# Kernel tuning notes

Hardware: AMD Instinct MI355X
Metric: run time of the kernel (lower is better)

## Reference

```python
import jax, jax.numpy as jnp
import numpy as np
import math

D, DK, DV = 1024, 128, 128
B, S = 4, 2048

def setup_inputs() -> dict:
    key = jax.random.key(0)
    k1, k2, k3, k4 = jax.random.split(key, 4)
    # xavier_normal std = sqrt(2/(fan_in+fan_out))
    std_qk = math.sqrt(2.0 / (D + DK))
    std_v = math.sqrt(2.0 / (D + DV))
    return {
        "X": jax.random.normal(k1, (B, S, D), dtype=jnp.float32),
        "W_q": jax.random.normal(k2, (D, DK), dtype=jnp.float32) * std_qk,
        "W_k": jax.random.normal(k3, (D, DK), dtype=jnp.float32) * std_qk,
        "W_v": jax.random.normal(k4, (D, DV), dtype=jnp.float32) * std_v,
    }

def reference(X, W_q, W_k, W_v):
    # Q,K,V projections: [B,S,D] @ [D,dk] -> [B,S,dk]
    Q = X @ W_q
    K = X @ W_k
    V = X @ W_v
    scale = 1.0 / math.sqrt(DK)
    # NOTE: original torch code calls A.masked_fill(...) without assigning the
    # result, so the causal mask is never actually applied. We replicate the
    # executed math: unmasked scaled dot-product attention.
    A = jnp.einsum("bqd,bkd->bqk", Q, K) * scale  # [B,S,S]
    A = jax.nn.softmax(A, axis=2)
    return jnp.einsum("bqk,bkv->bqv", A, V)  # [B,S,DV]
```

## Files before the change

### kernel.cpp

```cpp
#include <hip/hip_runtime.h>
#include <stdint.h>
#include <math.h>


typedef __attribute__((ext_vector_type(4))) float  f32x4;
typedef __attribute__((ext_vector_type(4))) short  s16x4;
typedef __attribute__((ext_vector_type(8))) short  s16x8;
typedef __attribute__((ext_vector_type(4))) float  fl4;

#define MFMA16(a,b,c) __builtin_amdgcn_mfma_f32_16x16x16bf16_1k(a,b,c,0,0,0)
#define MFMA32(a,b,c) __builtin_amdgcn_mfma_f32_16x16x32_bf16(a,b,c,0,0,0)

__device__ __forceinline__ short f2bf(float f){
  uint32_t u = __builtin_bit_cast(uint32_t, f);
  u = (u + 0x7FFFu + ((u >> 16) & 1u)) >> 16;
  return (short)u;
}

#define S_LEN   2048
#define D_IN    1024
#define D_HEAD  128
#define NROWS   8192
#define NSPLIT  4
#define KVB     64
#define KVPER   (S_LEN / NSPLIT)
#define NT      (KVPER / KVB)

#define WT_OFF  0u
#define Q_OFF   786432u
#define K_OFF   (786432u + 2097152u)
#define V_OFF   (786432u + 2u*2097152u)
#define OP_OFF  (786432u + 3u*2097152u)
#define ML_OFF  (OP_OFF + 16777216u)

__global__ __launch_bounds__(256) void wt3_kernel(
    const float* __restrict__ Wq, const float* __restrict__ Wk,
    const float* __restrict__ Wv, short* __restrict__ Wt){
  int i = blockIdx.x * 256 + threadIdx.x;
  int m = i >> 17;
  int r = i & 131071;
  int n = r >> 10;
  int k = r & 1023;
  const float* W = (m == 0) ? Wq : (m == 1 ? Wk : Wv);
  float v = W[k * D_HEAD + n];
  if (m == 0) v *= 0.08838834764831845f;
  Wt[i] = f2bf(v);
}

__global__ __launch_bounds__(256) void proj_kernel(
    const float* __restrict__ X, const short* __restrict__ Wt,
    short* __restrict__ Qo, short* __restrict__ Ko, short* __restrict__ Vt){
  const int mt  = blockIdx.x;
  const int mat = blockIdx.y;
  const short* Wm = Wt + mat * 131072;

  __shared__ short Xs[32][72];
  __shared__ short Ws[128][72];

  const int tid  = threadIdx.x;
  const int lane = tid & 63;
  const int wid  = tid >> 6;
  const int wm   = (wid >> 1) * 16;
  const int wn   = (wid & 1) * 64;
  const int lr   = lane & 15;
  const int lg8  = (lane >> 4) * 8;

  const f32x4 zero4 = {0.f, 0.f, 0.f, 0.f};
  f32x4 acc[4];
  #pragma unroll
  for (int n = 0; n < 4; n++) acc[n] = zero4;

  const int xr = tid >> 3, xc = (tid & 7) * 8;
  const int wr = tid >> 1, wc = (tid & 1) * 32;

  const float* xsrc0 = X + (size_t)(mt * 32 + xr) * D_IN + xc;
  const short* wsrc0 = Wm + (size_t)wr * D_IN + wc;

  fl4   xA, xB;
  s16x8 wR[4];

  xA = *(const fl4*)(xsrc0);
  xB = *(const fl4*)(xsrc0 + 4);
  #pragma unroll
  for (int j = 0; j < 4; j++) wR[j] = *(const s16x8*)(wsrc0 + 8 * j);

  #pragma unroll 1
  for (int kt = 0; kt < D_IN; kt += 64){
    {
      s16x8 v;
      #pragma unroll
      for (int j = 0; j < 4; j++){ v[j] = f2bf(xA[j]); v[j+4] = f2bf(xB[j]); }
      *(s16x8*)&Xs[xr][xc] = v;
      #pragma unroll
      for (int j = 0; j < 4; j++) *(s16x8*)&Ws[wr][wc + 8*j] = wR[j];
    }
    __syncthreads();

    if (kt + 64 < D_IN){
      xA = *(const fl4*)(xsrc0 + kt + 64);
      xB = *(const fl4*)(xsrc0 + kt + 68);
      #pragma unroll
      for (int j = 0; j < 4; j++) wR[j] = *(const s16x8*)(wsrc0 + kt + 64 + 8*j);
    }

    #pragma unroll
    for (int kc = 0; kc < 64; kc += 32){
      s16x8 af = *(const s16x8*)&Xs[wm + lr][kc + lg8];
      #pragma unroll
      for (int n = 0; n < 4; n++){
        s16x8 bf = *(const s16x8*)&Ws[wn + n*16 + lr][kc + lg8];
        acc[n] = MFMA32(af, bf, acc[n]);
      }
    }
    __syncthreads();
  }

  const int lg4 = (lane >> 4) * 4;
  if (mat < 2){
    short* dst = (mat == 0) ? Qo : Ko;
    #pragma unroll
    for (int n = 0; n < 4; n++){
      int col = wn + n*16 + lr;
      #pragma unroll
      for (int r = 0; r < 4; r++){
        int row = mt*32 + wm + lg4 + r;
        dst[(size_t)row * D_HEAD + col] = f2bf(acc[n][r]);
      }
    }
  } else {
    const int b  = (mt * 32) >> 11;
    const int s0 = (mt * 32) & 2047;
    #pragma unroll
    for (int n = 0; n < 4; n++){
      int dv = wn + n*16 + lr;
      int s  = s0 + wm + lg4;
      s16x4 v;
      #pragma unroll
      for (int r = 0; r < 4; r++) v[r] = f2bf(acc[n][r]);
      *(s16x4*)&Vt[((size_t)b * D_HEAD + dv) * S_LEN + s] = v;
    }
  }
}

__global__ __launch_bounds__(256) void flash_kernel(
    const short* __restrict__ Q, const short* __restrict__ K,
    const short* __restrict__ Vt, float* __restrict__ Opart,
    float* __restrict__ MLpart){
  const int sp = blockIdx.x;
  const int qt = blockIdx.y;
  const int b  = blockIdx.z;

  __shared__ short Ks[KVB][136];
  __shared__ short Vs[128][72];

  const int tid  = threadIdx.x;
  const int lane = tid & 63;
  const int w    = tid >> 6;
  const int lr   = lane & 15;
  const int lg   = lane >> 4;

  const int qrow = qt * 64 + w * 16 + lr;
  const short* Qr = Q + (size_t)(b * S_LEN + qrow) * D_HEAD + 8 * lg;
  s16x8 qf[4];
  #pragma unroll
  for (int c = 0; c < 4; c++) qf[c] = *(const s16x8*)(Qr + c * 32);

  const f32x4 zero4 = {0.f, 0.f, 0.f, 0.f};
  f32x4 o[8];
  #pragma unroll
  for (int t = 0; t < 8; t++) o[t] = zero4;
  float m_run = -INFINITY, l_run = 0.0f;

  const short* Kb = K  + (size_t)b * S_LEN * D_HEAD;
  const short* Vb = Vt + (size_t)b * D_HEAD * S_LEN;
  const int kr = tid >> 2, kc = (tid & 3) * 32;
  const int vr = tid >> 1, vc = (tid & 1) * 32;

  s16x8 kR[4], vR[4];
  const int kv_beg = sp * KVPER;

  {
    const short* ks = Kb + (size_t)(kv_beg + kr) * D_HEAD + kc;
    const short* vs = Vb + (size_t)vr * S_LEN + kv_beg + vc;
    #pragma unroll
    for (int j = 0; j < 4; j++){
      kR[j] = *(const s16x8*)(ks + 8*j);
      vR[j] = *(const s16x8*)(vs + 8*j);
    }
  }
  #pragma unroll
  for (int j = 0; j < 4; j++){
    *(s16x8*)&Ks[kr][kc + 8*j] = kR[j];
    *(s16x8*)&Vs[vr][vc + 8*j] = vR[j];
  }
  __syncthreads();

  #pragma unroll 1
  for (int it = 0; it < NT; ++it){
    if (it + 1 < NT){
      int kv0 = kv_beg + (it + 1) * KVB;
      const short* ks = Kb + (size_t)(kv0 + kr) * D_HEAD + kc;
      const short* vs = Vb + (size_t)vr * S_LEN + kv0 + vc;
      #pragma unroll
      for (int j = 0; j < 4; j++){
        kR[j] = *(const s16x8*)(ks + 8*j);
        vR[j] = *(const s16x8*)(vs + 8*j);
      }
    }

    f32x4 sa[4];
    #pragma unroll
    for (int t = 0; t < 4; t++) sa[t] = zero4;
    #pragma unroll
    for (int c = 0; c < 4; c++){
      #pragma unroll
      for (int t = 0; t < 4; t++){
        s16x8 ka = *(const s16x8*)&Ks[t*16 + lr][c*32 + 8*lg];
        sa[t] = MFMA32(ka, qf[c], sa[t]);
      }
    }

    float p[16]; float mx = -INFINITY;
    #pragma unroll
    for (int t = 0; t < 4; t++)
      #pragma unroll
      for (int r = 0; r < 4; r++){
        p[t*4 + r] = sa[t][r];
        mx = fmaxf(mx, sa[t][r]);
      }
    mx = fmaxf(mx, __shfl_xor(mx, 16));
    mx = fmaxf(mx, __shfl_xor(mx, 32));
    if (!__all(mx <= m_run + 8.0f)){
      float m_new = fmaxf(m_run, mx);
      float alpha = __expf(m_run - m_new);
      l_run *= alpha;
      #pragma unroll
      for (int t = 0; t < 8; t++) o[t] *= alpha;
      m_run = m_new;
    }
    float lsum = 0.0f;
    #pragma unroll
    for (int j = 0; j < 16; j++){ p[j] = __expf(p[j] - m_run); lsum += p[j]; }
    lsum += __shfl_xor(lsum, 16);
    lsum += __shfl_xor(lsum, 32);
    l_run += lsum;

    s16x4 pb[4];
    #pragma unroll
    for (int t = 0; t < 4; t++)
      #pragma unroll
      for (int r = 0; r < 4; r++) pb[t][r] = f2bf(p[t*4 + r]);

    #pragma unroll
    for (int dt = 0; dt < 8; dt++){
      #pragma unroll
      for (int t = 0; t < 4; t++){
        s16x4 va = *(const s16x4*)&Vs[dt*16 + lr][t*16 + 4*lg];
        o[dt] = MFMA16(va, pb[t], o[dt]);
      }
    }

    if (it + 1 < NT){
      __syncthreads();
      #pragma unroll
      for (int j = 0; j < 4; j++){
        *(s16x8*)&Ks[kr][kc + 8*j] = kR[j];
        *(s16x8*)&Vs[vr][vc + 8*j] = vR[j];
      }
      __syncthreads();
    }
  }

  const size_t grow = (size_t)b * S_LEN + qrow;
  float* Op = Opart + ((size_t)sp * NROWS + grow) * D_HEAD + 4 * lg;
  #pragma unroll
  for (int dt = 0; dt < 8; dt++)
    *(f32x4*)(Op + dt * 16) = o[dt];
  if (lg == 0){
    float* ml = MLpart + ((size_t)sp * NROWS + grow) * 2;
    ml[0] = m_run; ml[1] = l_run;
  }
}

__global__ __launch_bounds__(256) void merge_kernel(
    const float* __restrict__ Opart, const float* __restrict__ MLpart,
    float* __restrict__ out){
  int idx = blockIdx.x * 256 + threadIdx.x;
  int row = idx >> 7;
  float m[NSPLIT], l[NSPLIT];
  float M = -INFINITY;
  #pragma unroll
  for (int s = 0; s < NSPLIT; s++){
    m[s] = MLpart[((size_t)s * NROWS + row) * 2 + 0];
    l[s] = MLpart[((size_t)s * NROWS + row) * 2 + 1];
    M = fmaxf(M, m[s]);
  }
  float L = 0.f, val = 0.f;
  #pragma unroll
  for (int s = 0; s < NSPLIT; s++){
    float e = __expf(m[s] - M);
    L   += l[s] * e;
    val += Opart[(size_t)s * NROWS * D_HEAD + idx] * e;
  }
  out[idx] = val / L;
}

extern "C" void kernel_launch(void* const* d_in, const int* in_sizes, int n_in,
                              void* d_out, int out_size, void* d_ws, size_t ws_size,
                              hipStream_t stream){
  const float* X  = (const float*)d_in[0];
  const float* Wq = (const float*)d_in[1];
  const float* Wk = (const float*)d_in[2];
  const float* Wv = (const float*)d_in[3];
  char* ws = (char*)d_ws;
  short* Wt = (short*)(ws + WT_OFF);
  short* Qp = (short*)(ws + Q_OFF);
  short* Kp = (short*)(ws + K_OFF);
  short* Vt = (short*)(ws + V_OFF);
  float* Op = (float*)(ws + OP_OFF);
  float* Ml = (float*)(ws + ML_OFF);
  float* out = (float*)d_out;

  wt3_kernel  <<<dim3(1536),          dim3(256), 0, stream>>>(Wq, Wk, Wv, Wt);
  proj_kernel <<<dim3(256, 3),        dim3(256), 0, stream>>>(X, Wt, Qp, Kp, Vt);
  flash_kernel<<<dim3(NSPLIT, 32, 4), dim3(256), 0, stream>>>(Qp, Kp, Vt, Op, Ml);
  merge_kernel<<<dim3(4096),          dim3(256), 0, stream>>>(Op, Ml, out);
}
```

Before: 128.6 us.

## Double per-warp query rows in flash and projection, split KV into eight, use exp2

Each flash warp now handles two 16-row query fragments (128-row Q block), so every K and V fragment read from LDS feeds two MFMAs. KV is split eight ways to keep the grid size similar. The projection kernel likewise computes two M fragments per warp, reusing each W fragment twice. log2(e) is folded into the Q weight so softmax can use exp2f. s_setprio is raised around the MFMA sections. The cost is more accumulator registers per thread and twice the partial output traffic through the merge.

```diff
diff --git a/kernel.cpp b/kernel.cpp
--- a/kernel.cpp
+++ b/kernel.cpp
@@ -21,17 +21,21 @@
 #define D_IN    1024
 #define D_HEAD  128
 #define NROWS   8192
-#define NSPLIT  4
+#define NSPLIT  8
 #define KVB     64
 #define KVPER   (S_LEN / NSPLIT)
 #define NT      (KVPER / KVB)
+#define QBLK    128
 
 #define WT_OFF  0u
 #define Q_OFF   786432u
 #define K_OFF   (786432u + 2097152u)
 #define V_OFF   (786432u + 2u*2097152u)
 #define OP_OFF  (786432u + 3u*2097152u)
-#define ML_OFF  (OP_OFF + 16777216u)
+#define ML_OFF  (OP_OFF + 33554432u)
+
+#define LOG2E   1.4426950408889634f
+#define DEFER_TH 11.541560327111708f
 
 __global__ __launch_bounds__(256) void wt3_kernel(
     const float* __restrict__ Wq, const float* __restrict__ Wk,
@@ -43,7 +47,7 @@
   int k = r & 1023;
   const float* W = (m == 0) ? Wq : (m == 1 ? Wk : Wv);
   float v = W[k * D_HEAD + n];
-  if (m == 0) v *= 0.08838834764831845f;
+  if (m == 0) v *= 0.08838834764831845f * LOG2E;
   Wt[i] = f2bf(v);
 }
 
@@ -54,62 +58,75 @@
   const int mat = blockIdx.y;
   const short* Wm = Wt + mat * 131072;
 
-  __shared__ short Xs[32][72];
+  __shared__ short Xs[64][72];
   __shared__ short Ws[128][72];
 
   const int tid  = threadIdx.x;
   const int lane = tid & 63;
   const int wid  = tid >> 6;
-  const int wm   = (wid >> 1) * 16;
+  const int wm   = (wid >> 1) * 32;
   const int wn   = (wid & 1) * 64;
   const int lr   = lane & 15;
   const int lg8  = (lane >> 4) * 8;
 
   const f32x4 zero4 = {0.f, 0.f, 0.f, 0.f};
-  f32x4 acc[4];
-  #pragma unroll
-  for (int n = 0; n < 4; n++) acc[n] = zero4;
-
-  const int xr = tid >> 3, xc = (tid & 7) * 8;
+  f32x4 acc[2][4];
+  #pragma unroll
+  for (int mf = 0; mf < 2; mf++)
+    #pragma unroll
+    for (int n = 0; n < 4; n++) acc[mf][n] = zero4;
+
+  const int xr = tid >> 2, xc = (tid & 3) * 16;
   const int wr = tid >> 1, wc = (tid & 1) * 32;
 
-  const float* xsrc0 = X + (size_t)(mt * 32 + xr) * D_IN + xc;
+  const float* xsrc0 = X + (size_t)(mt * 64 + xr) * D_IN + xc;
   const short* wsrc0 = Wm + (size_t)wr * D_IN + wc;
 
-  fl4   xA, xB;
+  fl4   xA[4];
   s16x8 wR[4];
 
-  xA = *(const fl4*)(xsrc0);
-  xB = *(const fl4*)(xsrc0 + 4);
-  #pragma unroll
-  for (int j = 0; j < 4; j++) wR[j] = *(const s16x8*)(wsrc0 + 8 * j);
+  #pragma unroll
+  for (int j = 0; j < 4; j++){
+    xA[j] = *(const fl4*)(xsrc0 + 4 * j);
+    wR[j] = *(const s16x8*)(wsrc0 + 8 * j);
+  }
 
   #pragma unroll 1
   for (int kt = 0; kt < D_IN; kt += 64){
     {
-      s16x8 v;
-      #pragma unroll
-      for (int j = 0; j < 4; j++){ v[j] = f2bf(xA[j]); v[j+4] = f2bf(xB[j]); }
-      *(s16x8*)&Xs[xr][xc] = v;
+      s16x8 v0, v1;
+      #pragma unroll
+      for (int j = 0; j < 4; j++){
+        v0[j] = f2bf(xA[0][j]); v0[j+4] = f2bf(xA[1][j]);
+        v1[j] = f2bf(xA[2][j]); v1[j+4] = f2bf(xA[3][j]);
+      }
+      *(s16x8*)&Xs[xr][xc]     = v0;
+      *(s16x8*)&Xs[xr][xc + 8] = v1;
       #pragma unroll
       for (int j = 0; j < 4; j++) *(s16x8*)&Ws[wr][wc + 8*j] = wR[j];
     }
     __syncthreads();
 
     if (kt + 64 < D_IN){
-      xA = *(const fl4*)(xsrc0 + kt + 64);
-      xB = *(const fl4*)(xsrc0 + kt + 68);
-      #pragma unroll
-      for (int j = 0; j < 4; j++) wR[j] = *(const s16x8*)(wsrc0 + kt + 64 + 8*j);
+      #pragma unroll
+      for (int j = 0; j < 4; j++){
+        xA[j] = *(const fl4*)(xsrc0 + kt + 64 + 4*j);
+        wR[j] = *(const s16x8*)(wsrc0 + kt + 64 + 8*j);
+      }
     }
 
     #pragma unroll
     for (int kc = 0; kc < 64; kc += 32){
-      s16x8 af = *(const s16x8*)&Xs[wm + lr][kc + lg8];
+      s16x8 af[2];
+      #pragma unroll
+      for (int mf = 0; mf < 2; mf++)
+        af[mf] = *(const s16x8*)&Xs[wm + mf*16 + lr][kc + lg8];
       #pragma unroll
       for (int n = 0; n < 4; n++){
         s16x8 bf = *(const s16x8*)&Ws[wn + n*16 + lr][kc + lg8];
-        acc[n] = MFMA32(af, bf, acc[n]);
+        #pragma unroll
+        for (int mf = 0; mf < 2; mf++)
+          acc[mf][n] = MFMA32(af[mf], bf, acc[mf][n]);
       }
     }
     __syncthreads();
@@ -119,26 +136,30 @@
   if (mat < 2){
     short* dst = (mat == 0) ? Qo : Ko;
     #pragma unroll
-    for (int n = 0; n < 4; n++){
-      int col = wn + n*16 + lr;
-      #pragma unroll
-      for (int r = 0; r < 4; r++){
-        int row = mt*32 + wm + lg4 + r;
-        dst[(size_t)row * D_HEAD + col] = f2bf(acc[n][r]);
-      }
-    }
+    for (int mf = 0; mf < 2; mf++)
+      #pragma unroll
+      for (int n = 0; n < 4; n++){
+        int col = wn + n*16 + lr;
+        #pragma unroll
+        for (int r = 0; r < 4; r++){
+          int row = mt*64 + wm + mf*16 + lg4 + r;
+          dst[(size_t)row * D_HEAD + col] = f2bf(acc[mf][n][r]);
+        }
+      }
   } else {
-    const int b  = (mt * 32) >> 11;
-    const int s0 = (mt * 32) & 2047;
-    #pragma unroll
-    for (int n = 0; n < 4; n++){
-      int dv = wn + n*16 + lr;
-      int s  = s0 + wm + lg4;
-      s16x4 v;
-      #pragma unroll
-      for (int r = 0; r < 4; r++) v[r] = f2bf(acc[n][r]);
-      *(s16x4*)&Vt[((size_t)b * D_HEAD + dv) * S_LEN + s] = v;
-    }
+    const int b  = (mt * 64) >> 11;
+    const int s0 = (mt * 64) & 2047;
+    #pragma unroll
+    for (int mf = 0; mf < 2; mf++)
+      #pragma unroll
+      for (int n = 0; n < 4; n++){
+        int dv = wn + n*16 + lr;
+        int s  = s0 + wm + mf*16 + lg4;
+        s16x4 v;
+        #pragma unroll
+        for (int r = 0; r < 4; r++) v[r] = f2bf(acc[mf][n][r]);
+        *(s16x4*)&Vt[((size_t)b * D_HEAD + dv) * S_LEN + s] = v;
+      }
   }
 }
 
@@ -159,17 +180,23 @@
   const int lr   = lane & 15;
   const int lg   = lane >> 4;
 
-  const int qrow = qt * 64 + w * 16 + lr;
-  const short* Qr = Q + (size_t)(b * S_LEN + qrow) * D_HEAD + 8 * lg;
-  s16x8 qf[4];
-  #pragma unroll
-  for (int c = 0; c < 4; c++) qf[c] = *(const s16x8*)(Qr + c * 32);
+  const int qrow0 = qt * QBLK + w * 32 + lr;
+  const short* Qr = Q + (size_t)(b * S_LEN + qrow0) * D_HEAD + 8 * lg;
+  s16x8 qf[2][4];
+  #pragma unroll
+  for (int qi = 0; qi < 2; qi++)
+    #pragma unroll
+    for (int c = 0; c < 4; c++)
+      qf[qi][c] = *(const s16x8*)(Qr + qi * 16 * D_HEAD + c * 32);
 
   const f32x4 zero4 = {0.f, 0.f, 0.f, 0.f};
-  f32x4 o[8];
-  #pragma unroll
-  for (int t = 0; t < 8; t++) o[t] = zero4;
-  float m_run = -INFINITY, l_run = 0.0f;
+  f32x4 o[2][8];
+  #pragma unroll
+  for (int qi = 0; qi < 2; qi++)
+    #pragma unroll
+    for (int t = 0; t < 8; t++) o[qi][t] = zero4;
+  float m_run[2] = {-INFINITY, -INFINITY};
+  float l_run[2] = {0.0f, 0.0f};
 
   const short* Kb = K  + (size_t)b * S_LEN * D_HEAD;
   const short* Vb = Vt + (size_t)b * D_HEAD * S_LEN;
@@ -208,57 +235,66 @@
       }
     }
 
-    f32x4 sa[4];
-    #pragma unroll
-    for (int t = 0; t < 4; t++) sa[t] = zero4;
+    f32x4 sa[2][4];
+    #pragma unroll
+    for (int qi = 0; qi < 2; qi++)
+      #pragma unroll
+      for (int t = 0; t < 4; t++) sa[qi][t] = zero4;
+    __builtin_amdgcn_s_setprio(1);
     #pragma unroll
     for (int c = 0; c < 4; c++){
       #pragma unroll
       for (int t = 0; t < 4; t++){
         s16x8 ka = *(const s16x8*)&Ks[t*16 + lr][c*32 + 8*lg];
-        sa[t] = MFMA32(ka, qf[c], sa[t]);
-      }
-    }
-
-    float p[16]; float mx = -INFINITY;
-    #pragma unroll
-    for (int t = 0; t < 4; t++)
-      #pragma unroll
-      for (int r = 0; r < 4; r++){
-        p[t*4 + r] = sa[t][r];
-        mx = fmaxf(mx, sa[t][r]);
-      }
-    mx = fmaxf(mx, __shfl_xor(mx, 16));
-    mx = fmaxf(mx, __shfl_xor(mx, 32));
-    if (!__all(mx <= m_run + 8.0f)){
-      float m_new = fmaxf(m_run, mx);
-      float alpha = __expf(m_run - m_new);
-      l_run *= alpha;
-      #pragma unroll
-      for (int t = 0; t < 8; t++) o[t] *= alpha;
-      m_run = m_new;
-    }
-    float lsum = 0.0f;
-    #pragma unroll
-    for (int j = 0; j < 16; j++){ p[j] = __expf(p[j] - m_run); lsum += p[j]; }
-    lsum += __shfl_xor(lsum, 16);
-    lsum += __shfl_xor(lsum, 32);
-    l_run += lsum;
-
-    s16x4 pb[4];
-    #pragma unroll
-    for (int t = 0; t < 4; t++)
-      #pragma unroll
-      for (int r = 0; r < 4; r++) pb[t][r] = f2bf(p[t*4 + r]);
-
+        sa[0][t] = MFMA32(ka, qf[0][c], sa[0][t]);
+        sa[1][t] = MFMA32(ka, qf[1][c], sa[1][t]);
+      }
+    }
+    __builtin_amdgcn_s_setprio(0);
+
+    s16x4 pb[2][4];
+    #pragma unroll
+    for (int qi = 0; qi < 2; qi++){
+      float mx = -INFINITY;
+      #pragma unroll
+      for (int t = 0; t < 4; t++)
+        #pragma unroll
+        for (int r = 0; r < 4; r++) mx = fmaxf(mx, sa[qi][t][r]);
+      mx = fmaxf(mx, __shfl_xor(mx, 16));
+      mx = fmaxf(mx, __shfl_xor(mx, 32));
+      if (!__all(mx <= m_run[qi] + DEFER_TH)){
+        float m_new = fmaxf(m_run[qi], mx);
+        float alpha = exp2f(m_run[qi] - m_new);
+        l_run[qi] *= alpha;
+        #pragma unroll
+        for (int t = 0; t < 8; t++) o[qi][t] *= alpha;
+        m_run[qi] = m_new;
+      }
+      float lsum = 0.0f;
+      #pragma unroll
+      for (int t = 0; t < 4; t++)
+        #pragma unroll
+        for (int r = 0; r < 4; r++){
+          float e = exp2f(sa[qi][t][r] - m_run[qi]);
+          pb[qi][t][r] = f2bf(e);
+          lsum += e;
+        }
+      lsum += __shfl_xor(lsum, 16);
+      lsum += __shfl_xor(lsum, 32);
+      l_run[qi] += lsum;
+    }
+
+    __builtin_amdgcn_s_setprio(1);
     #pragma unroll
     for (int dt = 0; dt < 8; dt++){
       #pragma unroll
       for (int t = 0; t < 4; t++){
         s16x4 va = *(const s16x4*)&Vs[dt*16 + lr][t*16 + 4*lg];
-        o[dt] = MFMA16(va, pb[t], o[dt]);
-      }
-    }
+        o[0][dt] = MFMA16(va, pb[0][t], o[0][dt]);
+        o[1][dt] = MFMA16(va, pb[1][t], o[1][dt]);
+      }
+    }
+    __builtin_amdgcn_s_setprio(0);
 
     if (it + 1 < NT){
       __syncthreads();
@@ -271,14 +307,18 @@
     }
   }
 
-  const size_t grow = (size_t)b * S_LEN + qrow;
-  float* Op = Opart + ((size_t)sp * NROWS + grow) * D_HEAD + 4 * lg;
-  #pragma unroll
-  for (int dt = 0; dt < 8; dt++)
-    *(f32x4*)(Op + dt * 16) = o[dt];
-  if (lg == 0){
-    float* ml = MLpart + ((size_t)sp * NROWS + grow) * 2;
-    ml[0] = m_run; ml[1] = l_run;
+  const int lg4 = lg * 4;
+  #pragma unroll
+  for (int qi = 0; qi < 2; qi++){
+    const size_t grow = (size_t)b * S_LEN + qrow0 + qi * 16;
+    float* Op = Opart + ((size_t)sp * NROWS + grow) * D_HEAD + lg4;
+    #pragma unroll
+    for (int dt = 0; dt < 8; dt++)
+      *(f32x4*)(Op + dt * 16) = o[qi][dt];
+    if (lg == 0){
+      float* ml = MLpart + ((size_t)sp * NROWS + grow) * 2;
+      ml[0] = m_run[qi]; ml[1] = l_run[qi];
+    }
   }
 }
 
@@ -298,7 +338,7 @@
   float L = 0.f, val = 0.f;
   #pragma unroll
   for (int s = 0; s < NSPLIT; s++){
-    float e = __expf(m[s] - M);
+    float e = exp2f(m[s] - M);
     L   += l[s] * e;
     val += Opart[(size_t)s * NROWS * D_HEAD + idx] * e;
   }
@@ -321,8 +361,8 @@
   float* Ml = (float*)(ws + ML_OFF);
   float* out = (float*)d_out;
 
-  wt3_kernel  <<<dim3(1536),          dim3(256), 0, stream>>>(Wq, Wk, Wv, Wt);
-  proj_kernel <<<dim3(256, 3),        dim3(256), 0, stream>>>(X, Wt, Qp, Kp, Vt);
-  flash_kernel<<<dim3(NSPLIT, 32, 4), dim3(256), 0, stream>>>(Qp, Kp, Vt, Op, Ml);
-  merge_kernel<<<dim3(4096),          dim3(256), 0, stream>>>(Op, Ml, out);
-}
+  wt3_kernel  <<<dim3(1536),           dim3(256), 0, stream>>>(Wq, Wk, Wv, Wt);
+  proj_kernel <<<dim3(128, 3),         dim3(256), 0, stream>>>(X, Wt, Qp, Kp, Vt);
+  flash_kernel<<<dim3(NSPLIT, 16, 4),  dim3(256), 0, stream>>>(Qp, Kp, Vt, Op, Ml);
+  merge_kernel<<<dim3(4096),           dim3(256), 0, stream>>>(Op, Ml, out);
+}
```

Result: slower. 141.1 us (+9.8%).
